# Optimization experiments

Measured on AMD Instinct MI355X. Metric: run time of the kernel, lower is better.

The kernel has to match this reference:

```python
import jax, jax.numpy as jnp
import numpy as np

D_MODEL = 2048
N_Q_HEADS = 32
N_KV_HEADS = 8
HEAD_DIM = D_MODEL // N_Q_HEADS  # 64
KV_DIM = HEAD_DIM * N_KV_HEADS   # 512
B, S = 2, 2048


def setup_inputs() -> dict:
    key = jax.random.key(0)
    ks = jax.random.split(key, 11)
    sc_d = 1.0 / np.sqrt(D_MODEL)
    return {
        "query": jax.random.normal(ks[0], (B, S, D_MODEL), jnp.float32),
        "key":   jax.random.normal(ks[1], (B, S, D_MODEL), jnp.float32),
        "value": jax.random.normal(ks[2], (B, S, D_MODEL), jnp.float32),
        "Wq": jax.random.normal(ks[3], (D_MODEL, D_MODEL), jnp.float32) * sc_d,
        "bq": jnp.zeros((D_MODEL,), jnp.float32),
        "Wk": jax.random.normal(ks[4], (D_MODEL, KV_DIM), jnp.float32) * sc_d,
        "bk": jnp.zeros((KV_DIM,), jnp.float32),
        "Wv": jax.random.normal(ks[5], (D_MODEL, KV_DIM), jnp.float32) * sc_d,
        "bv": jnp.zeros((KV_DIM,), jnp.float32),
        "Wo": jax.random.normal(ks[6], (D_MODEL, D_MODEL), jnp.float32) * sc_d,
        "bo": jnp.zeros((D_MODEL,), jnp.float32),
    }


def reference(query, key, value, Wq, bq, Wk, bk, Wv, bv, Wo, bo):
    b, s, _ = query.shape
    g = N_Q_HEADS // N_KV_HEADS  # num groups
    # projections
    Q = query @ Wq + bq                      # [b, s, d_model]
    K = key @ Wk + bk                        # [b, s, kv_dim]
    V = value @ Wv + bv                      # [b, s, kv_dim]
    # split heads. Torch code splits Q into groups of num_kv_heads heads,
    # and each group broadcasts per-head against the Hkv KV heads, i.e.
    # query head (grp*Hkv + j) attends against kv head j.
    Q = Q.reshape(b, s, g, N_KV_HEADS, HEAD_DIM)  # [b, s, g, hkv, d]
    K = K.reshape(b, s, N_KV_HEADS, HEAD_DIM)     # [b, s, hkv, d]
    V = V.reshape(b, s, N_KV_HEADS, HEAD_DIM)
    scale = 1.0 / jnp.sqrt(jnp.float32(HEAD_DIM))
    scores = jnp.einsum('bsghd,bthd->bghst', Q, K) * scale  # [b,g,hkv,s,s]
    attn = jax.nn.softmax(scores, axis=-1)
    out = jnp.einsum('bghst,bthd->bsghd', attn, V)          # [b,s,g,hkv,d]
    # concat over groups then heads == original head order (g major, hkv minor)
    out = out.reshape(b, s, D_MODEL)
    return out @ Wo + bo
```

## Files before the change

### kernel.cpp

```cpp
#include <hip/hip_runtime.h>
#include <cstdint>

typedef _Float16 half4 __attribute__((ext_vector_type(4)));
typedef _Float16 half8 __attribute__((ext_vector_type(8)));
typedef _Float16 half16 __attribute__((ext_vector_type(16)));
typedef float f32x4 __attribute__((ext_vector_type(4)));
typedef float f32x16 __attribute__((ext_vector_type(16)));

#define L2E 1.44269504088896340736f

__device__ __forceinline__ void gl16(const void* g, void* l) {
  __builtin_amdgcn_global_load_lds(
      (const __attribute__((address_space(1))) void*)g,
      (__attribute__((address_space(3))) void*)l, 16, 0, 0);
}

__device__ __forceinline__ uint32_t pk2(float a, float b) {
  return __builtin_bit_cast(uint32_t, __builtin_amdgcn_cvt_pkrtz(a, b));
}

__device__ __forceinline__ void plswap(uint32_t& x, uint32_t& y) {
  auto r = __builtin_amdgcn_permlane32_swap((int)x, (int)y, false, false);
  x = (uint32_t)r[0];
  y = (uint32_t)r[1];
}

__device__ __forceinline__ f32x16 zero16() {
  f32x16 z;
  #pragma unroll
  for (int r = 0; r < 16; ++r) z[r] = 0.0f;
  return z;
}

__global__ __launch_bounds__(256) void transpose_w_all(
    const float* __restrict__ Wq, const float* __restrict__ Wk,
    const float* __restrict__ Wv, const float* __restrict__ Wo,
    _Float16* __restrict__ WqkvT, _Float16* __restrict__ WoT)
{
  int id = blockIdx.x;
  const float* src;
  _Float16* dst;
  int N, tx, ty;
  if (id < 4096)      { src = Wq; dst = WqkvT;                        N = 2048; tx = id & 63; ty = id >> 6; }
  else if (id < 5120) { id -= 4096; src = Wk; dst = WqkvT + (size_t)2048 * 2048; N = 512; tx = id & 15; ty = id >> 4; }
  else if (id < 6144) { id -= 5120; src = Wv; dst = WqkvT + (size_t)2560 * 2048; N = 512; tx = id & 15; ty = id >> 4; }
  else                { id -= 6144; src = Wo; dst = WoT;              N = 2048; tx = id & 63; ty = id >> 6; }
  const int n0 = tx * 32, k0 = ty * 32;
  __shared__ float t[32][33];
  #pragma unroll
  for (int i = 0; i < 4; ++i)
    t[threadIdx.y + i * 8][threadIdx.x] =
        src[(size_t)(k0 + threadIdx.y + i * 8) * N + n0 + threadIdx.x];
  __syncthreads();
  #pragma unroll
  for (int i = 0; i < 4; ++i)
    dst[(size_t)(n0 + threadIdx.y + i * 8) * 2048 + k0 + threadIdx.x] =
        (_Float16)t[threadIdx.x][threadIdx.y + i * 8];
}

__global__ __launch_bounds__(256) void transpose_v(
    const _Float16* __restrict__ QKV, _Float16* __restrict__ VT)
{
  const int bh = blockIdx.z;
  const int bb = bh >> 3, h = bh & 7;
  const int t0 = blockIdx.x * 32, d0 = blockIdx.y * 32;
  __shared__ _Float16 t[32][33];
  const _Float16* src = QKV + (size_t)(bb * 2048) * 3072 + 2560 + h * 64;
  #pragma unroll
  for (int i = 0; i < 4; ++i)
    t[threadIdx.y + i * 8][threadIdx.x] =
        src[(size_t)(t0 + threadIdx.y + i * 8) * 3072 + d0 + threadIdx.x];
  __syncthreads();
  _Float16* dst = VT + ((size_t)(bb * 8 + h) * 64) * 2048;
  #pragma unroll
  for (int i = 0; i < 4; ++i)
    dst[(size_t)(d0 + threadIdx.y + i * 8) * 2048 + t0 + threadIdx.x] =
        t[threadIdx.x][threadIdx.y + i * 8];
}

template<int MODE>
__global__ __launch_bounds__(512, MODE + 1) void gemm256(
    const float* __restrict__ Fq, const float* __restrict__ Fk, const float* __restrict__ Fv,
    const _Float16* __restrict__ Ah,
    const _Float16* __restrict__ Bt,
    const float* __restrict__ bias0, const float* __restrict__ bias1, const float* __restrict__ bias2,
    _Float16* __restrict__ Ch, float* __restrict__ Cf)
{
  constexpr int K = 2048;
  constexpr int N = (MODE == 0) ? 3072 : 2048;
  constexpr int NB = N / 256;
  constexpr int BM = (MODE == 0) ? 256 : 128;
  constexpr int G = (4096 / BM) * NB;
  constexpr int ABYTES = BM * 64;
  constexpr int BUF = ABYTES + 16384;
  constexpr int MT = BM / 32;

  const int wg = blockIdx.x;
  const int work = (wg & 7) * (G / 8) + (wg >> 3);
  const int m0 = (work / NB) * BM;
  const int n0 = (work % NB) * 256;

  const float* Af = Fq;
  if constexpr (MODE == 0) { if (n0 >= 2560) Af = Fv; else if (n0 >= 2048) Af = Fk; }

  const int tid = threadIdx.x;
  const int lane = tid & 63;
  const int w = tid >> 6;
  const int wr = w >> 2;
  const int wc = w & 3;
  const int lo = lane & 15, hi = lane >> 4;

  __shared__ __align__(1024) char smem[3 * BUF];

  f32x4 acc[MT][4];
  #pragma unroll
  for (int mt = 0; mt < MT; ++mt)
    #pragma unroll
    for (int nt = 0; nt < 4; ++nt)
      acc[mt][nt] = (f32x4){0.f, 0.f, 0.f, 0.f};

  const _Float16* pB = Bt + (size_t)(n0 + w * 32 + (lane >> 2)) * K + (lane & 3) * 8;
  const int dstB = ABYTES + w * 2048;

  const float* pA32 = nullptr;
  const _Float16* pA16 = nullptr;
  if constexpr (MODE == 0)
    pA32 = Af + (size_t)(m0 + w * 32 + (lane >> 2)) * K + (lane & 3) * 8;
  else
    pA16 = Ah + (size_t)(m0 + w * 16 + (lane >> 2)) * K + (lane & 3) * 8;

  if constexpr (MODE == 0) {
    f32x4 q00 = *(const f32x4*)pA32;
    f32x4 q01 = *(const f32x4*)(pA32 + 4);
    f32x4 q02 = *(const f32x4*)(pA32 + (size_t)16 * K);
    f32x4 q03 = *(const f32x4*)(pA32 + (size_t)16 * K + 4);
    gl16(pB, smem + dstB);
    gl16(pB + (size_t)16 * K, smem + dstB + 1024);
    f32x4 q10 = *(const f32x4*)(pA32 + 32);
    f32x4 q11 = *(const f32x4*)(pA32 + 36);
    f32x4 q12 = *(const f32x4*)(pA32 + (size_t)16 * K + 32);
    f32x4 q13 = *(const f32x4*)(pA32 + (size_t)16 * K + 36);
    gl16(pB + 32, smem + BUF + dstB);
    gl16(pB + 32 + (size_t)16 * K, smem + BUF + dstB + 1024);
    pA32 += 64; pB += 64;
    asm volatile("s_waitcnt vmcnt(0)" ::: "memory");
    char* wp0 = smem + w * 2048 + lane * 16;
    union { uint32_t u[4]; half8 h; } cv;
    cv.u[0] = pk2(q00[0], q00[1]); cv.u[1] = pk2(q00[2], q00[3]);
    cv.u[2] = pk2(q01[0], q01[1]); cv.u[3] = pk2(q01[2], q01[3]);
    *(half8*)wp0 = cv.h;
    cv.u[0] = pk2(q02[0], q02[1]); cv.u[1] = pk2(q02[2], q02[3]);
    cv.u[2] = pk2(q03[0], q03[1]); cv.u[3] = pk2(q03[2], q03[3]);
    *(half8*)(wp0 + 1024) = cv.h;
    char* wp1 = smem + BUF + w * 2048 + lane * 16;
    cv.u[0] = pk2(q10[0], q10[1]); cv.u[1] = pk2(q10[2], q10[3]);
    cv.u[2] = pk2(q11[0], q11[1]); cv.u[3] = pk2(q11[2], q11[3]);
    *(half8*)wp1 = cv.h;
    cv.u[0] = pk2(q12[0], q12[1]); cv.u[1] = pk2(q12[2], q12[3]);
    cv.u[2] = pk2(q13[0], q13[1]); cv.u[3] = pk2(q13[2], q13[3]);
    *(half8*)(wp1 + 1024) = cv.h;
    asm volatile("s_waitcnt lgkmcnt(0)" ::: "memory");
    __builtin_amdgcn_s_barrier();
  } else {
    gl16(pA16, smem + w * 1024);
    gl16(pB, smem + dstB);
    gl16(pB + (size_t)16 * K, smem + dstB + 1024);
    gl16(pA16 + 32, smem + BUF + w * 1024);
    gl16(pB + 32, smem + BUF + dstB);
    gl16(pB + 32 + (size_t)16 * K, smem + BUF + dstB + 1024);
    pA16 += 64; pB += 64;
    asm volatile("s_waitcnt vmcnt(3)" ::: "memory");
    __builtin_amdgcn_s_barrier();
  }

  const int abase = (wr * (BM / 2) + lo) * 64 + hi * 16;
  const int bbase = ABYTES + (wc * 64 + lo) * 64 + hi * 16;

  int c = 0;
  for (int t = 0; t < 64; ++t) {
    int c1 = c + 1; if (c1 == 3) c1 = 0;
    int c2 = c1 + 1; if (c2 == 3) c2 = 0;
    const bool st = (t < 62);
    f32x4 ar0, ar1, ar2, ar3;
    if (st) {
      char* bp_ = smem + c2 * BUF;
      if constexpr (MODE == 0) {
        ar0 = *(const f32x4*)pA32;
        ar1 = *(const f32x4*)(pA32 + 4);
        ar2 = *(const f32x4*)(pA32 + (size_t)16 * K);
        ar3 = *(const f32x4*)(pA32 + (size_t)16 * K + 4);
        pA32 += 32;
      } else {
        gl16(pA16, bp_ + w * 1024);
        pA16 += 32;
      }
      gl16(pB, bp_ + dstB);
      gl16(pB + (size_t)16 * K, bp_ + dstB + 1024);
      pB += 32;
    }

    const char* bc = smem + c * BUF;
    half8 af[MT], bf[4];
    #pragma unroll
    for (int mt = 0; mt < MT; ++mt) af[mt] = *(const half8*)(bc + abase + mt * 1024);
    #pragma unroll
    for (int nt = 0; nt < 4; ++nt) bf[nt] = *(const half8*)(bc + bbase + nt * 1024);

    __builtin_amdgcn_s_setprio(1);
    #pragma unroll
    for (int mt = 0; mt < MT; ++mt)
      #pragma unroll
      for (int nt = 0; nt < 4; ++nt)
        acc[mt][nt] = __builtin_amdgcn_mfma_f32_16x16x32_f16(af[mt], bf[nt], acc[mt][nt], 0, 0, 0);
    __builtin_amdgcn_s_setprio(0);

    if (st) {
      if constexpr (MODE == 0) {
        asm volatile("s_waitcnt vmcnt(2)" ::: "memory");
        char* wp = smem + c2 * BUF + w * 2048 + lane * 16;
        union { uint32_t u[4]; half8 h; } cv;
        cv.u[0] = pk2(ar0[0], ar0[1]); cv.u[1] = pk2(ar0[2], ar0[3]);
        cv.u[2] = pk2(ar1[0], ar1[1]); cv.u[3] = pk2(ar1[2], ar1[3]);
        *(half8*)wp = cv.h;
        cv.u[0] = pk2(ar2[0], ar2[1]); cv.u[1] = pk2(ar2[2], ar2[3]);
        cv.u[2] = pk2(ar3[0], ar3[1]); cv.u[3] = pk2(ar3[2], ar3[3]);
        *(half8*)(wp + 1024) = cv.h;
      } else {
        asm volatile("s_waitcnt vmcnt(3)" ::: "memory");
      }
    } else if (t == 62) {
      asm volatile("s_waitcnt vmcnt(0)" ::: "memory");
    }
    if (t < 63) {
      if constexpr (MODE == 0) asm volatile("s_waitcnt lgkmcnt(0)" ::: "memory");
      __builtin_amdgcn_s_barrier();
    }
    c = c1;
  }

  float* T = (float*)smem;
  const int tr = tid >> 4;
  const int sc = tid & 15;
  #pragma unroll
  for (int mp = 0; mp < MT; ++mp) {
    __syncthreads();
    #pragma unroll
    for (int nt = 0; nt < 4; ++nt)
      #pragma unroll
      for (int r = 0; r < 4; ++r)
        T[(wr * 16 + 4 * hi + r) * 256 + wc * 64 + nt * 16 + lo] = acc[mp][nt][r];
    __syncthreads();
    const int grow = m0 + (tr >> 4) * (BM / 2) + mp * 16 + (tr & 15);
    const int gcol = n0 + sc * 16;
    const float* Trow = T + tr * 256 + sc * 16;
    float4 v[4];
    #pragma unroll
    for (int q = 0; q < 4; ++q) v[q] = ((const float4*)Trow)[q];
    const float* bp = bias0;
    int cb = gcol;
    if constexpr (MODE == 0) {
      if (gcol >= 2560) { bp = bias2; cb = gcol - 2560; }
      else if (gcol >= 2048) { bp = bias1; cb = gcol - 2048; }
    }
    float4 bvv[4];
    #pragma unroll
    for (int q = 0; q < 4; ++q) bvv[q] = ((const float4*)(bp + cb))[q];
    if constexpr (MODE == 0) {
      half16 o;
      #pragma unroll
      for (int q = 0; q < 4; ++q) {
        o[4 * q + 0] = (_Float16)(v[q].x + bvv[q].x);
        o[4 * q + 1] = (_Float16)(v[q].y + bvv[q].y);
        o[4 * q + 2] = (_Float16)(v[q].z + bvv[q].z);
        o[4 * q + 3] = (_Float16)(v[q].w + bvv[q].w);
      }
      *(half16*)(Ch + (size_t)grow * N + gcol) = o;
    } else {
      float* dstp = Cf + (size_t)grow * N + gcol;
      #pragma unroll
      for (int q = 0; q < 4; ++q) {
        float4 ov = {v[q].x + bvv[q].x, v[q].y + bvv[q].y, v[q].z + bvv[q].z, v[q].w + bvv[q].w};
        ((float4*)dstp)[q] = ov;
      }
    }
  }
}

__global__ __launch_bounds__(256, 5) void attn_fwd4(
    const _Float16* __restrict__ QKV, const _Float16* __restrict__ VT,
    _Float16* __restrict__ AO)
{
  const int wg = blockIdx.x;
  const int work = (wg & 7) * 128 + (wg >> 3);
  const int bh = work >> 6;
  const int b = bh >> 3, h = bh & 7;
  const int rem = work & 63;
  const int qh = (rem >> 4) * 8 + h;
  const int qt = rem & 15;

  const int tid = threadIdx.x;
  const int lane = tid & 63;
  const int w = tid >> 6;
  const int l31 = lane & 31;
  const int hi5 = lane >> 5;
  const int r7 = l31 & 7;

  __shared__ __align__(1024) char sm[2][2][8192];

  const _Float16 QSC = (_Float16)(0.125f * L2E);
  const int qrow0 = b * 2048 + qt * 128 + w * 32 + l31;
  half8 qf[4];
  {
    const _Float16* qp = QKV + (size_t)qrow0 * 3072 + qh * 64 + hi5 * 8;
    #pragma unroll
    for (int s = 0; s < 4; ++s) {
      half8 q = *(const half8*)(qp + s * 16);
      #pragma unroll
      for (int e = 0; e < 8; ++e) q[e] = q[e] * QSC;
      qf[s] = q;
    }
  }

  const int li = lane >> 3;
  const int lc = lane & 7;
  const int kslot = lc ^ li;
  const int w16li = w * 16 + li;
  const _Float16* Ksrc = QKV + ((size_t)(b * 2048 + w16li)) * 3072 + 2048 + h * 64 + kslot * 8;
  const _Float16* Vsrc = VT + ((size_t)(b * 8 + h) * 64 + w16li) * 2048 + kslot * 8;

  f32x16 oa[2];
  oa[0] = zero16();
  oa[1] = zero16();
  float lreg = 0.f;

  {
    char* kd = &sm[0][0][0] + w * 2048;
    char* vd = &sm[0][1][0] + w * 2048;
    gl16(Ksrc, kd);
    gl16(Ksrc + (size_t)8 * 3072, kd + 1024);
    gl16(Vsrc, vd);
    gl16(Vsrc + (size_t)8 * 2048, vd + 1024);
  }
  __syncthreads();

  int cur = 0;
  for (int t = 0; t < 32; ++t) {
    if (t < 31) {
      const int t0 = (t + 1) * 64;
      char* kd = &sm[cur ^ 1][0][0] + w * 2048;
      char* vd = &sm[cur ^ 1][1][0] + w * 2048;
      const _Float16* kg = Ksrc + (size_t)t0 * 3072;
      const _Float16* vg = Vsrc + t0;
      gl16(kg, kd);
      gl16(kg + (size_t)8 * 3072, kd + 1024);
      gl16(vg, vd);
      gl16(vg + (size_t)8 * 2048, vd + 1024);
    }

    const char* Kb = &sm[cur][0][0];
    const char* Vb = &sm[cur][1][0];

    uint32_t pw[4][4];
    float ps = 0.f;
    #pragma unroll
    for (int j = 0; j < 2; ++j) {
      f32x16 sa = zero16();
      const int kr = j * 32 + l31;
      __builtin_amdgcn_s_setprio(1);
      #pragma unroll
      for (int s = 0; s < 4; ++s) {
        half8 kf = *(const half8*)(Kb + kr * 128 + (((2 * s + hi5) ^ r7) << 4));
        sa = __builtin_amdgcn_mfma_f32_32x32x16_f16(kf, qf[s], sa, 0, 0, 0);
      }
      __builtin_amdgcn_s_setprio(0);
      #pragma unroll
      for (int r = 0; r < 16; ++r) {
        const float p = __builtin_amdgcn_exp2f(sa[r]);
        sa[r] = p;
        ps += p;
      }
      #pragma unroll
      for (int hf = 0; hf < 2; ++hf) {
        const int rb = hf * 8;
        uint32_t w0 = pk2(sa[rb + 0], sa[rb + 1]);
        uint32_t w1 = pk2(sa[rb + 2], sa[rb + 3]);
        uint32_t w2 = pk2(sa[rb + 4], sa[rb + 5]);
        uint32_t w3 = pk2(sa[rb + 6], sa[rb + 7]);
        plswap(w0, w2);
        plswap(w1, w3);
        const int s = 2 * j + hf;
        pw[s][0] = w0; pw[s][1] = w1; pw[s][2] = w2; pw[s][3] = w3;
      }
    }
    ps += __shfl_xor(ps, 32);
    lreg += ps;

    __builtin_amdgcn_s_setprio(1);
    #pragma unroll
    for (int s = 0; s < 4; ++s) {
      union { uint32_t u[4]; half8 h; } p0;
      #pragma unroll
      for (int u = 0; u < 4; ++u) p0.u[u] = pw[s][u];
      #pragma unroll
      for (int i = 0; i < 2; ++i) {
        const int vr = i * 32 + l31;
        half8 vf = *(const half8*)(Vb + vr * 128 + (((2 * s + hi5) ^ r7) << 4));
        oa[i] = __builtin_amdgcn_mfma_f32_32x32x16_f16(vf, p0.h, oa[i], 0, 0, 0);
      }
    }
    __builtin_amdgcn_s_setprio(0);

    __syncthreads();
    cur ^= 1;
  }

  {
    const float inv = 1.0f / lreg;
    #pragma unroll
    for (int i = 0; i < 2; ++i) {
      _Float16* dst = AO + (size_t)qrow0 * 2048 + qh * 64 + i * 32 + hi5 * 4;
      #pragma unroll
      for (int q = 0; q < 4; ++q) {
        union { uint32_t u[2]; half4 h4; } o;
        o.u[0] = pk2(oa[i][4 * q + 0] * inv, oa[i][4 * q + 1] * inv);
        o.u[1] = pk2(oa[i][4 * q + 2] * inv, oa[i][4 * q + 3] * inv);
        *(half4*)(dst + 8 * q) = o.h4;
      }
    }
  }
}

extern "C" void kernel_launch(void* const* d_in, const int* in_sizes, int n_in,
                              void* d_out, int out_size, void* d_ws, size_t ws_size,
                              hipStream_t stream) {
  const float* query = (const float*)d_in[0];
  const float* key   = (const float*)d_in[1];
  const float* value = (const float*)d_in[2];
  const float* Wq = (const float*)d_in[3];
  const float* bq = (const float*)d_in[4];
  const float* Wk = (const float*)d_in[5];
  const float* bk = (const float*)d_in[6];
  const float* Wv = (const float*)d_in[7];
  const float* bv = (const float*)d_in[8];
  const float* Wo = (const float*)d_in[9];
  const float* bo = (const float*)d_in[10];
  float* out = (float*)d_out;

  char* ws = (char*)d_ws;
  _Float16* WqkvT = (_Float16*)(ws + 50331648);
  _Float16* WoT   = (_Float16*)(ws + 62914560);
  _Float16* QKVh  = (_Float16*)(ws + 71303168);
  _Float16* VT    = (_Float16*)(ws + 96468992);
  _Float16* aoh   = (_Float16*)(ws + 100663296);

  transpose_w_all<<<10240, dim3(32, 8), 0, stream>>>(Wq, Wk, Wv, Wo, WqkvT, WoT);
  gemm256<0><<<192, 512, 0, stream>>>(query, key, value, nullptr, WqkvT,
                                      bq, bk, bv, QKVh, nullptr);
  transpose_v<<<dim3(64, 2, 16), dim3(32, 8), 0, stream>>>(QKVh, VT);
  attn_fwd4<<<1024, 256, 0, stream>>>(QKVh, VT, aoh);
  gemm256<1><<<256, 512, 0, stream>>>(nullptr, nullptr, nullptr, aoh, WoT,
                                      bo, nullptr, nullptr, nullptr, out);
}
```

Before: 230.0 us.

## Shrink QKV projection GEMM tile to 128 rows and deepen fp32 A prefetch

The QKV projection GEMM now uses 128x256 tiles instead of 256x256, launching 384 workgroups instead of 192 and allowing two blocks per CU. This is meant to fill more of the CUs and shorten the tail. The fp32 A-operand loads are restructured to prefetch one extra k-step ahead in registers, with adjusted vmcnt waits, so the convert-and-store to LDS no longer waits on loads issued in the same iteration. In exchange, each tile reuses the weights over fewer rows, so there is more global traffic for B, and the wait-count pipeline becomes more delicate.

```diff
diff --git a/kernel.cpp b/kernel.cpp
--- a/kernel.cpp
+++ b/kernel.cpp
@@ -79,7 +79,7 @@
 }
 
 template<int MODE>
-__global__ __launch_bounds__(512, MODE + 1) void gemm256(
+__global__ __launch_bounds__(512, 2) void gemm128(
     const float* __restrict__ Fq, const float* __restrict__ Fk, const float* __restrict__ Fv,
     const _Float16* __restrict__ Ah,
     const _Float16* __restrict__ Bt,
@@ -89,15 +89,12 @@
   constexpr int K = 2048;
   constexpr int N = (MODE == 0) ? 3072 : 2048;
   constexpr int NB = N / 256;
-  constexpr int BM = (MODE == 0) ? 256 : 128;
-  constexpr int G = (4096 / BM) * NB;
-  constexpr int ABYTES = BM * 64;
-  constexpr int BUF = ABYTES + 16384;
-  constexpr int MT = BM / 32;
+  constexpr int G = 32 * NB;
+  constexpr int BUF = 8192 + 16384;
 
   const int wg = blockIdx.x;
   const int work = (wg & 7) * (G / 8) + (wg >> 3);
-  const int m0 = (work / NB) * BM;
+  const int m0 = (work / NB) * 128;
   const int n0 = (work % NB) * 256;
 
   const float* Af = Fq;
@@ -112,128 +109,124 @@
 
   __shared__ __align__(1024) char smem[3 * BUF];
 
-  f32x4 acc[MT][4];
-  #pragma unroll
-  for (int mt = 0; mt < MT; ++mt)
+  f32x4 acc[4][4];
+  #pragma unroll
+  for (int mt = 0; mt < 4; ++mt)
     #pragma unroll
     for (int nt = 0; nt < 4; ++nt)
       acc[mt][nt] = (f32x4){0.f, 0.f, 0.f, 0.f};
 
   const _Float16* pB = Bt + (size_t)(n0 + w * 32 + (lane >> 2)) * K + (lane & 3) * 8;
-  const int dstB = ABYTES + w * 2048;
+  const size_t bstep = (size_t)16 * K;
+  const int dstB = 8192 + w * 2048;
 
   const float* pA32 = nullptr;
   const _Float16* pA16 = nullptr;
   if constexpr (MODE == 0)
-    pA32 = Af + (size_t)(m0 + w * 32 + (lane >> 2)) * K + (lane & 3) * 8;
+    pA32 = Af + (size_t)(m0 + w * 16 + (lane >> 2)) * K + (lane & 3) * 8;
   else
     pA16 = Ah + (size_t)(m0 + w * 16 + (lane >> 2)) * K + (lane & 3) * 8;
+  const int dstA = w * 1024;
+
+  f32x4 ar0, ar1;
 
   if constexpr (MODE == 0) {
-    f32x4 q00 = *(const f32x4*)pA32;
-    f32x4 q01 = *(const f32x4*)(pA32 + 4);
-    f32x4 q02 = *(const f32x4*)(pA32 + (size_t)16 * K);
-    f32x4 q03 = *(const f32x4*)(pA32 + (size_t)16 * K + 4);
-    gl16(pB, smem + dstB);
-    gl16(pB + (size_t)16 * K, smem + dstB + 1024);
-    f32x4 q10 = *(const f32x4*)(pA32 + 32);
-    f32x4 q11 = *(const f32x4*)(pA32 + 36);
-    f32x4 q12 = *(const f32x4*)(pA32 + (size_t)16 * K + 32);
-    f32x4 q13 = *(const f32x4*)(pA32 + (size_t)16 * K + 36);
-    gl16(pB + 32, smem + BUF + dstB);
-    gl16(pB + 32 + (size_t)16 * K, smem + BUF + dstB + 1024);
-    pA32 += 64; pB += 64;
-    asm volatile("s_waitcnt vmcnt(0)" ::: "memory");
-    char* wp0 = smem + w * 2048 + lane * 16;
+    f32x4 p00 = *(const f32x4*)pA32;
+    f32x4 p01 = *(const f32x4*)(pA32 + 4);
+    f32x4 p10 = *(const f32x4*)(pA32 + 32);
+    f32x4 p11 = *(const f32x4*)(pA32 + 36);
+    ar0 = *(const f32x4*)(pA32 + 64);
+    ar1 = *(const f32x4*)(pA32 + 68);
+    pA32 += 96;
+    gl16(pB,         smem + dstB);        gl16(pB + bstep,      smem + dstB + 1024);
+    gl16(pB + 32,    smem + BUF + dstB);  gl16(pB + 32 + bstep, smem + BUF + dstB + 1024);
+    pB += 64;
+    asm volatile("s_waitcnt vmcnt(4)" ::: "memory");
     union { uint32_t u[4]; half8 h; } cv;
-    cv.u[0] = pk2(q00[0], q00[1]); cv.u[1] = pk2(q00[2], q00[3]);
-    cv.u[2] = pk2(q01[0], q01[1]); cv.u[3] = pk2(q01[2], q01[3]);
+    char* wp0 = smem + dstA + lane * 16;
+    cv.u[0] = pk2(p00[0], p00[1]); cv.u[1] = pk2(p00[2], p00[3]);
+    cv.u[2] = pk2(p01[0], p01[1]); cv.u[3] = pk2(p01[2], p01[3]);
     *(half8*)wp0 = cv.h;
-    cv.u[0] = pk2(q02[0], q02[1]); cv.u[1] = pk2(q02[2], q02[3]);
-    cv.u[2] = pk2(q03[0], q03[1]); cv.u[3] = pk2(q03[2], q03[3]);
-    *(half8*)(wp0 + 1024) = cv.h;
-    char* wp1 = smem + BUF + w * 2048 + lane * 16;
-    cv.u[0] = pk2(q10[0], q10[1]); cv.u[1] = pk2(q10[2], q10[3]);
-    cv.u[2] = pk2(q11[0], q11[1]); cv.u[3] = pk2(q11[2], q11[3]);
+    char* wp1 = smem + BUF + dstA + lane * 16;
+    cv.u[0] = pk2(p10[0], p10[1]); cv.u[1] = pk2(p10[2], p10[3]);
+    cv.u[2] = pk2(p11[0], p11[1]); cv.u[3] = pk2(p11[2], p11[3]);
     *(half8*)wp1 = cv.h;
-    cv.u[0] = pk2(q12[0], q12[1]); cv.u[1] = pk2(q12[2], q12[3]);
-    cv.u[2] = pk2(q13[0], q13[1]); cv.u[3] = pk2(q13[2], q13[3]);
-    *(half8*)(wp1 + 1024) = cv.h;
+    asm volatile("s_waitcnt vmcnt(2)" ::: "memory");
     asm volatile("s_waitcnt lgkmcnt(0)" ::: "memory");
     __builtin_amdgcn_s_barrier();
   } else {
-    gl16(pA16, smem + w * 1024);
-    gl16(pB, smem + dstB);
-    gl16(pB + (size_t)16 * K, smem + dstB + 1024);
-    gl16(pA16 + 32, smem + BUF + w * 1024);
-    gl16(pB + 32, smem + BUF + dstB);
-    gl16(pB + 32 + (size_t)16 * K, smem + BUF + dstB + 1024);
+    gl16(pA16,      smem + dstA);
+    gl16(pB,        smem + dstB);        gl16(pB + bstep,      smem + dstB + 1024);
+    gl16(pA16 + 32, smem + BUF + dstA);
+    gl16(pB + 32,   smem + BUF + dstB);  gl16(pB + 32 + bstep, smem + BUF + dstB + 1024);
     pA16 += 64; pB += 64;
     asm volatile("s_waitcnt vmcnt(3)" ::: "memory");
     __builtin_amdgcn_s_barrier();
   }
 
-  const int abase = (wr * (BM / 2) + lo) * 64 + hi * 16;
-  const int bbase = ABYTES + (wc * 64 + lo) * 64 + hi * 16;
+  const int abase = (wr * 64 + lo) * 64 + hi * 16;
+  const int bbase = 8192 + (wc * 64 + lo) * 64 + hi * 16;
 
   int c = 0;
   for (int t = 0; t < 64; ++t) {
     int c1 = c + 1; if (c1 == 3) c1 = 0;
     int c2 = c1 + 1; if (c2 == 3) c2 = 0;
-    const bool st = (t < 62);
-    f32x4 ar0, ar1, ar2, ar3;
-    if (st) {
-      char* bp_ = smem + c2 * BUF;
-      if constexpr (MODE == 0) {
+    char* bp_ = smem + c2 * BUF;
+
+    if constexpr (MODE == 0) {
+      if (t <= 61) {
+        asm volatile("s_waitcnt vmcnt(2)" ::: "memory");
+        union { uint32_t u[4]; half8 h; } cv;
+        cv.u[0] = pk2(ar0[0], ar0[1]); cv.u[1] = pk2(ar0[2], ar0[3]);
+        cv.u[2] = pk2(ar1[0], ar1[1]); cv.u[3] = pk2(ar1[2], ar1[3]);
+        *(half8*)(bp_ + dstA + lane * 16) = cv.h;
+      }
+      if (t <= 60) {
         ar0 = *(const f32x4*)pA32;
         ar1 = *(const f32x4*)(pA32 + 4);
-        ar2 = *(const f32x4*)(pA32 + (size_t)16 * K);
-        ar3 = *(const f32x4*)(pA32 + (size_t)16 * K + 4);
         pA32 += 32;
-      } else {
-        gl16(pA16, bp_ + w * 1024);
-        pA16 += 32;
-      }
-      gl16(pB, bp_ + dstB);
-      gl16(pB + (size_t)16 * K, bp_ + dstB + 1024);
-      pB += 32;
+      }
+      if (t <= 61) {
+        gl16(pB, bp_ + dstB);
+        gl16(pB + bstep, bp_ + dstB + 1024);
+        pB += 32;
+      }
+    } else {
+      if (t < 62) {
+        gl16(pA16, bp_ + dstA);
+        gl16(pB, bp_ + dstB);
+        gl16(pB + bstep, bp_ + dstB + 1024);
+        pA16 += 32; pB += 32;
+      }
     }
 
     const char* bc = smem + c * BUF;
-    half8 af[MT], bf[4];
-    #pragma unroll
-    for (int mt = 0; mt < MT; ++mt) af[mt] = *(const half8*)(bc + abase + mt * 1024);
+    half8 af[4], bf[4];
+    #pragma unroll
+    for (int mt = 0; mt < 4; ++mt) af[mt] = *(const half8*)(bc + abase + mt * 1024);
     #pragma unroll
     for (int nt = 0; nt < 4; ++nt) bf[nt] = *(const half8*)(bc + bbase + nt * 1024);
 
     __builtin_amdgcn_s_setprio(1);
     #pragma unroll
-    for (int mt = 0; mt < MT; ++mt)
+    for (int mt = 0; mt < 4; ++mt)
       #pragma unroll
       for (int nt = 0; nt < 4; ++nt)
         acc[mt][nt] = __builtin_amdgcn_mfma_f32_16x16x32_f16(af[mt], bf[nt], acc[mt][nt], 0, 0, 0);
     __builtin_amdgcn_s_setprio(0);
 
-    if (st) {
-      if constexpr (MODE == 0) {
-        asm volatile("s_waitcnt vmcnt(2)" ::: "memory");
-        char* wp = smem + c2 * BUF + w * 2048 + lane * 16;
-        union { uint32_t u[4]; half8 h; } cv;
-        cv.u[0] = pk2(ar0[0], ar0[1]); cv.u[1] = pk2(ar0[2], ar0[3]);
-        cv.u[2] = pk2(ar1[0], ar1[1]); cv.u[3] = pk2(ar1[2], ar1[3]);
-        *(half8*)wp = cv.h;
-        cv.u[0] = pk2(ar2[0], ar2[1]); cv.u[1] = pk2(ar2[2], ar2[3]);
-        cv.u[2] = pk2(ar3[0], ar3[1]); cv.u[3] = pk2(ar3[2], ar3[3]);
-        *(half8*)(wp + 1024) = cv.h;
-      } else {
-        asm volatile("s_waitcnt vmcnt(3)" ::: "memory");
-      }
-    } else if (t == 62) {
-      asm volatile("s_waitcnt vmcnt(0)" ::: "memory");
-    }
-    if (t < 63) {
-      if constexpr (MODE == 0) asm volatile("s_waitcnt lgkmcnt(0)" ::: "memory");
-      __builtin_amdgcn_s_barrier();
+    if constexpr (MODE == 0) {
+      if (t <= 60)      asm volatile("s_waitcnt vmcnt(4)" ::: "memory");
+      else if (t == 61) asm volatile("s_waitcnt vmcnt(2)" ::: "memory");
+      else if (t == 62) asm volatile("s_waitcnt vmcnt(0)" ::: "memory");
+      if (t < 63) {
+        asm volatile("s_waitcnt lgkmcnt(0)" ::: "memory");
+        __builtin_amdgcn_s_barrier();
+      }
+    } else {
+      if (t < 62)       asm volatile("s_waitcnt vmcnt(3)" ::: "memory");
+      else if (t == 62) asm volatile("s_waitcnt vmcnt(0)" ::: "memory");
+      if (t < 63) __builtin_amdgcn_s_barrier();
     }
     c = c1;
   }
@@ -242,7 +235,7 @@
   const int tr = tid >> 4;
   const int sc = tid & 15;
   #pragma unroll
-  for (int mp = 0; mp < MT; ++mp) {
+  for (int mp = 0; mp < 4; ++mp) {
     __syncthreads();
     #pragma unroll
     for (int nt = 0; nt < 4; ++nt)
@@ -250,7 +243,7 @@
       for (int r = 0; r < 4; ++r)
         T[(wr * 16 + 4 * hi + r) * 256 + wc * 64 + nt * 16 + lo] = acc[mp][nt][r];
     __syncthreads();
-    const int grow = m0 + (tr >> 4) * (BM / 2) + mp * 16 + (tr & 15);
+    const int grow = m0 + (tr >> 4) * 64 + mp * 16 + (tr & 15);
     const int gcol = n0 + sc * 16;
     const float* Trow = T + tr * 256 + sc * 16;
     float4 v[4];
@@ -454,10 +447,10 @@
   _Float16* aoh   = (_Float16*)(ws + 100663296);
 
   transpose_w_all<<<10240, dim3(32, 8), 0, stream>>>(Wq, Wk, Wv, Wo, WqkvT, WoT);
-  gemm256<0><<<192, 512, 0, stream>>>(query, key, value, nullptr, WqkvT,
+  gemm128<0><<<384, 512, 0, stream>>>(query, key, value, nullptr, WqkvT,
                                       bq, bk, bv, QKVh, nullptr);
   transpose_v<<<dim3(64, 2, 16), dim3(32, 8), 0, stream>>>(QKVh, VT);
   attn_fwd4<<<1024, 256, 0, stream>>>(QKVh, VT, aoh);
-  gemm256<1><<<256, 512, 0, stream>>>(nullptr, nullptr, nullptr, aoh, WoT,
+  gemm128<1><<<256, 512, 0, stream>>>(nullptr, nullptr, nullptr, aoh, WoT,
                                       bo, nullptr, nullptr, nullptr, out);
 }
```

Result: no change. 229.2 us (-0.4%).
